# Kernel optimization log

Measured on AMD Instinct MI355X. Metric: run time of the kernel, lower is better.

## Reference

```python
import jax, jax.numpy as jnp
import numpy as np

INTEGRAL_RESOLUTION = 0.03  # matches self.integral_resolution

S, H, E, G, F = 4096, 3, 512, 3334, 1  # samples, heads, max events, grid points, formulas


def setup_inputs() -> dict:
    key = jax.random.key(0)
    k1, k2, k3, k4, k5, k6 = jax.random.split(key, 6)
    event_features = jax.random.uniform(k1, (S, H, E, F), dtype=jnp.float32)
    event_mask = jax.random.randint(k2, (S, H, E), 0, 2).astype(bool)
    grid_features = jax.random.uniform(k3, (S, H, G, F), dtype=jnp.float32)
    weights = jax.random.normal(k4, (H, F), dtype=jnp.float32)
    bases = jax.random.normal(k5, (H,), dtype=jnp.float32)
    effects = jnp.ones((H, F), dtype=jnp.float32)  # formula effect is +/-1
    return {
        "event_features": event_features,
        "event_mask": event_mask,
        "grid_features": grid_features,
        "weights": weights,
        "bases": bases,
        "effects": effects,
    }


def reference(event_features, event_mask, grid_features, weights, bases, effects):
    # intensity(t, h) = exp(base_h + sum_f w_{h,f} * feature_f(t) * effect_{h,f})
    w_eff = weights * effects  # [H, F]
    # log-intensity at event times: [S, H, E]
    ev_logit = bases[None, :, None] + jnp.einsum('shef,hf->she', event_features, w_eff)
    # log-intensity on the integral grid: [S, H, G]
    gr_logit = bases[None, :, None] + jnp.einsum('shgf,hf->shg', grid_features, w_eff)
    # sum of log(intensity) over valid events (log(exp(x)) = x)
    log_sum = jnp.sum(jnp.where(event_mask, ev_logit, jnp.zeros((), ev_logit.dtype)))
    # Riemann integral of intensity over [0, T_max]
    integral = jnp.asarray(INTEGRAL_RESOLUTION, gr_logit.dtype) * jnp.sum(jnp.exp(gr_logit))
    return log_sum - integral
```

## Files before the change

### kernel.cpp

```cpp
#include <hip/hip_runtime.h>

constexpr int S = 4096;
constexpr int H = 3;
constexpr int E = 512;
constexpr int G = 3334;
constexpr float RES = 0.03f;
constexpr float LOG2E = 1.44269504088896340736f;

constexpr int NBLK = 2048;
constexpr int BT   = 256;
constexpr int NF4G = S * H * G / 4;
constexpr int GPB  = NF4G / NBLK;
constexpr int NF4E = S * H * E / 4;
constexpr int EPB  = NF4E / NBLK;
constexpr int TAIL_T = GPB - 19 * BT;

#if __has_builtin(__builtin_amdgcn_exp2f)
#define EXP2(x) __builtin_amdgcn_exp2f(x)
#else
#define EXP2(x) exp2f(x)
#endif

__device__ __forceinline__ float quad_exp(int fidx, float4 y,
                                          float c0, float c1, float c2,
                                          float v0, float v1, float v2) {
    int j = fidx * 4;
    int q = j / G;
    int r = j - q * G;
    int m = q - (q / 3) * 3;
    int hB = (m == 2) ? 0 : (m + 1);
    float cA = (m == 0) ? c0 : ((m == 1) ? c1 : c2);
    float vA = (m == 0) ? v0 : ((m == 1) ? v1 : v2);
    float cB = (hB == 0) ? c0 : ((hB == 1) ? c1 : c2);
    float vB = (hB == 0) ? v0 : ((hB == 1) ? v1 : v2);
    int lim = G - r;
    float s;
    s  = EXP2(cA + vA * y.x);
    s += EXP2(((1 >= lim) ? cB : cA) + ((1 >= lim) ? vB : vA) * y.y);
    s += EXP2(((2 >= lim) ? cB : cA) + ((2 >= lim) ? vB : vA) * y.z);
    s += EXP2(((3 >= lim) ? cB : cA) + ((3 >= lim) ? vB : vA) * y.w);
    return s;
}

__global__ __launch_bounds__(256) void logic_model_kernel(
    const float* __restrict__ ev,
    const int*   __restrict__ mask,
    const float* __restrict__ gr,
    const float* __restrict__ w,
    const float* __restrict__ bases,
    const float* __restrict__ eff,
    float* __restrict__ out)
{
    const float b0 = bases[0], b1 = bases[1], b2 = bases[2];
    const float w0 = w[0] * eff[0], w1 = w[1] * eff[1], w2 = w[2] * eff[2];
    const float c0 = b0 * LOG2E, c1 = b1 * LOG2E, c2 = b2 * LOG2E;
    const float v0 = w0 * LOG2E, v1 = w1 * LOG2E, v2 = w2 * LOG2E;

    const int t = threadIdx.x;
    const float4* ev4 = (const float4*)ev;
    const int4*   m4  = (const int4*)mask;
    const float4* gr4 = (const float4*)gr;

    const int ebase = blockIdx.x * EPB + t;
    const int gbase = blockIdx.x * GPB;

    float4 p1x[3]; int4 p1m[3];
    #pragma unroll
    for (int u = 0; u < 3; ++u) {
        p1x[u] = ev4[ebase + u * BT];
        p1m[u] = m4[ebase + u * BT];
    }
    float4 buf[4][4];
    #pragma unroll
    for (int g = 0; g < 3; ++g) {
        #pragma unroll
        for (int u = 0; u < 4; ++u) {
            int slot = 4 * g + u;
            buf[g][u] = gr4[gbase + t + slot * BT];
        }
    }
    __builtin_amdgcn_sched_barrier(0);

    float acc_ev = 0.f;
    #pragma unroll
    for (int u = 0; u < 3; ++u) {
        int row = (ebase + u * BT) >> 7;
        int h = row - (row / 3) * 3;
        float bb = (h == 0) ? b0 : ((h == 1) ? b1 : b2);
        float ww = (h == 0) ? w0 : ((h == 1) ? w1 : w2);
        float4 x = p1x[u]; int4 m = p1m[u];
        if (m.x) acc_ev += bb + ww * x.x;
        if (m.y) acc_ev += bb + ww * x.y;
        if (m.z) acc_ev += bb + ww * x.z;
        if (m.w) acc_ev += bb + ww * x.w;
    }
    __builtin_amdgcn_sched_barrier(0);

    float acc_gr = 0.f;
    #pragma unroll
    for (int b = 0; b < 5; ++b) {
        if (b + 3 < 5) {
            int g = b + 3;
            #pragma unroll
            for (int u = 0; u < 4; ++u) {
                int slot = 4 * g + u;
                int pos = t + slot * BT;
                int idx = gbase + ((slot == 19 && t >= TAIL_T) ? 0 : pos);
                buf[g & 3][u] = gr4[idx];
            }
        }
        __builtin_amdgcn_sched_barrier(0);
        #pragma unroll
        for (int u = 0; u < 4; ++u) {
            int slot = 4 * b + u;
            int pos = t + slot * BT;
            bool valid = (slot < 19) || (t < TAIL_T);
            int fidx = gbase + (valid ? pos : 0);
            float s = quad_exp(fidx, buf[b & 3][u], c0, c1, c2, v0, v1, v2);
            acc_gr += valid ? s : 0.f;
        }
        __builtin_amdgcn_sched_barrier(0);
    }

    float v = acc_ev - RES * acc_gr;

    #pragma unroll
    for (int off = 32; off > 0; off >>= 1)
        v += __shfl_down(v, off, 64);

    __shared__ float sdata[4];
    const int wave = threadIdx.x >> 6;
    const int lane = threadIdx.x & 63;
    if (lane == 0) sdata[wave] = v;
    __syncthreads();
    if (threadIdx.x == 0) {
        float s = sdata[0] + sdata[1] + sdata[2] + sdata[3];
        atomicAdd(out, s);
    }
}

extern "C" void kernel_launch(void* const* d_in, const int* in_sizes, int n_in,
                              void* d_out, int out_size, void* d_ws, size_t ws_size,
                              hipStream_t stream) {
    const float* ev    = (const float*)d_in[0];
    const int*   mask  = (const int*)  d_in[1];
    const float* gr    = (const float*)d_in[2];
    const float* wgt   = (const float*)d_in[3];
    const float* bases = (const float*)d_in[4];
    const float* eff   = (const float*)d_in[5];
    float* out = (float*)d_out;

    hipMemsetAsync(out, 0, sizeof(float), stream);

    logic_model_kernel<<<NBLK, BT, 0, stream>>>(ev, mask, gr, wgt, bases, eff, out);
}
```

Measured before the change: 270.2 us.

## Repartition work into exact per-thread tiles across more blocks, drop manual pipelining

Launches 3334 blocks so each thread handles exactly 12 grid float4s and, for the first 3072 blocks, 2 event float4s. This removes tail masking and the hand-rolled multi-stage load buffering with sched barriers. The aim is simpler code, more parallelism and fewer wasted predicated lanes. In exchange it gives up explicit load/compute overlap ordering, and adds more atomics and load imbalance from the event work.

```diff
diff --git a/kernel.cpp b/kernel.cpp
--- a/kernel.cpp
+++ b/kernel.cpp
@@ -7,13 +7,16 @@
 constexpr float RES = 0.03f;
 constexpr float LOG2E = 1.44269504088896340736f;
 
-constexpr int NBLK = 2048;
 constexpr int BT   = 256;
+constexpr int NBLK = 3334;
 constexpr int NF4G = S * H * G / 4;
-constexpr int GPB  = NF4G / NBLK;
+constexpr int GQ   = NF4G / (NBLK * BT);
 constexpr int NF4E = S * H * E / 4;
-constexpr int EPB  = NF4E / NBLK;
-constexpr int TAIL_T = GPB - 19 * BT;
+constexpr int EBLK = 3072;
+constexpr int EQ   = NF4E / (EBLK * BT);
+
+static_assert(NBLK * BT * GQ == NF4G, "grid partition exact");
+static_assert(EBLK * BT * EQ == NF4E, "event partition exact");
 
 #if __has_builtin(__builtin_amdgcn_exp2f)
 #define EXP2(x) __builtin_amdgcn_exp2f(x)
@@ -57,69 +60,45 @@
     const float v0 = w0 * LOG2E, v1 = w1 * LOG2E, v2 = w2 * LOG2E;
 
     const int t = threadIdx.x;
+    const int b = blockIdx.x;
     const float4* ev4 = (const float4*)ev;
     const int4*   m4  = (const int4*)mask;
     const float4* gr4 = (const float4*)gr;
 
-    const int ebase = blockIdx.x * EPB + t;
-    const int gbase = blockIdx.x * GPB;
-
-    float4 p1x[3]; int4 p1m[3];
-    #pragma unroll
-    for (int u = 0; u < 3; ++u) {
-        p1x[u] = ev4[ebase + u * BT];
-        p1m[u] = m4[ebase + u * BT];
-    }
-    float4 buf[4][4];
-    #pragma unroll
-    for (int g = 0; g < 3; ++g) {
-        #pragma unroll
-        for (int u = 0; u < 4; ++u) {
-            int slot = 4 * g + u;
-            buf[g][u] = gr4[gbase + t + slot * BT];
-        }
-    }
-    __builtin_amdgcn_sched_barrier(0);
-
-    float acc_ev = 0.f;
-    #pragma unroll
-    for (int u = 0; u < 3; ++u) {
-        int row = (ebase + u * BT) >> 7;
-        int h = row - (row / 3) * 3;
-        float bb = (h == 0) ? b0 : ((h == 1) ? b1 : b2);
-        float ww = (h == 0) ? w0 : ((h == 1) ? w1 : w2);
-        float4 x = p1x[u]; int4 m = p1m[u];
-        if (m.x) acc_ev += bb + ww * x.x;
-        if (m.y) acc_ev += bb + ww * x.y;
-        if (m.z) acc_ev += bb + ww * x.z;
-        if (m.w) acc_ev += bb + ww * x.w;
+    const bool do_ev = (b < EBLK);
+    const int ebase = b * (EQ * BT) + t;
+    float4 ex0 = {0,0,0,0}, ex1 = {0,0,0,0};
+    int4   em0 = {0,0,0,0}, em1 = {0,0,0,0};
+    if (do_ev) {
+        ex0 = ev4[ebase];      em0 = m4[ebase];
+        ex1 = ev4[ebase + BT]; em1 = m4[ebase + BT];
     }
     __builtin_amdgcn_sched_barrier(0);
 
     float acc_gr = 0.f;
+    const int gbase = b * (GQ * BT) + t;
     #pragma unroll
-    for (int b = 0; b < 5; ++b) {
-        if (b + 3 < 5) {
-            int g = b + 3;
-            #pragma unroll
-            for (int u = 0; u < 4; ++u) {
-                int slot = 4 * g + u;
-                int pos = t + slot * BT;
-                int idx = gbase + ((slot == 19 && t >= TAIL_T) ? 0 : pos);
-                buf[g & 3][u] = gr4[idx];
-            }
+    for (int u = 0; u < GQ; ++u) {
+        int fidx = gbase + u * BT;
+        acc_gr += quad_exp(fidx, gr4[fidx], c0, c1, c2, v0, v1, v2);
+    }
+
+    float acc_ev = 0.f;
+    if (do_ev) {
+        #pragma unroll
+        for (int u = 0; u < EQ; ++u) {
+            int fidx = ebase + u * BT;
+            int row = fidx >> 7;
+            int h = row - (row / 3) * 3;
+            float bb = (h == 0) ? b0 : ((h == 1) ? b1 : b2);
+            float ww = (h == 0) ? w0 : ((h == 1) ? w1 : w2);
+            float4 x = (u == 0) ? ex0 : ex1;
+            int4   m = (u == 0) ? em0 : em1;
+            if (m.x) acc_ev += bb + ww * x.x;
+            if (m.y) acc_ev += bb + ww * x.y;
+            if (m.z) acc_ev += bb + ww * x.z;
+            if (m.w) acc_ev += bb + ww * x.w;
         }
-        __builtin_amdgcn_sched_barrier(0);
-        #pragma unroll
-        for (int u = 0; u < 4; ++u) {
-            int slot = 4 * b + u;
-            int pos = t + slot * BT;
-            bool valid = (slot < 19) || (t < TAIL_T);
-            int fidx = gbase + (valid ? pos : 0);
-            float s = quad_exp(fidx, buf[b & 3][u], c0, c1, c2, v0, v1, v2);
-            acc_gr += valid ? s : 0.f;
-        }
-        __builtin_amdgcn_sched_barrier(0);
     }
 
     float v = acc_ev - RES * acc_gr;
@@ -129,11 +108,11 @@
         v += __shfl_down(v, off, 64);
 
     __shared__ float sdata[4];
-    const int wave = threadIdx.x >> 6;
-    const int lane = threadIdx.x & 63;
+    const int wave = t >> 6;
+    const int lane = t & 63;
     if (lane == 0) sdata[wave] = v;
     __syncthreads();
-    if (threadIdx.x == 0) {
+    if (t == 0) {
         float s = sdata[0] + sdata[1] + sdata[2] + sdata[3];
         atomicAdd(out, s);
     }
```

New measurement: 272.3 us. No clear change (+0.8%).
